# Kernel tuning notes

Hardware: AMD Instinct MI355X
Metric: run time of the kernel (lower is better)

## Reference

```python
import jax, jax.numpy as jnp
import numpy as np

B, S, D, H = 4, 2048, 1024, 16
HD = D // H


def setup_inputs() -> dict:
    key = jax.random.key(0)
    ks = jax.random.split(key, 12)
    inp = {
        'query': jax.random.normal(ks[0], (B, S, D), jnp.float32),
        'key': jax.random.normal(ks[1], (B, S, D), jnp.float32),
        'value': jax.random.normal(ks[2], (B, S, D), jnp.float32),
        'mask': jnp.ones((B, 1, 1, S), jnp.bool_),
        # nn.Linear weights are [out, in]; y = x @ W.T + b
        'Wq': jax.random.normal(ks[3], (D, D), jnp.float32) * 0.02,
        'bq': jnp.zeros((D,), jnp.float32),
        'Wk': jax.random.normal(ks[4], (D, D), jnp.float32) * 0.02,
        'bk': jnp.zeros((D,), jnp.float32),
        'Wv': jax.random.normal(ks[5], (D, D), jnp.float32) * 0.02,
        'bv': jnp.zeros((D,), jnp.float32),
        'Wo': jax.random.normal(ks[6], (D, D), jnp.float32) * 0.02,
        'bo': jnp.zeros((D,), jnp.float32),
    }
    return inp


def reference(query, key, value, mask, Wq, bq, Wk, bk, Wv, bv, Wo, bo):
    scale = 1.0 / np.sqrt(HD).astype(np.float32)

    def proj(x, W, b):
        # [B,S,D] -> [B,H,S,HD]
        y = x @ W.T + b
        return y.reshape(B, S, H, HD).transpose(0, 2, 1, 3)

    q = proj(query, Wq, bq)
    k = proj(key, Wk, bk)
    v = proj(value, Wv, bv)
    # scores: [B,H,S,S]
    scores = jnp.einsum('bhqd,bhkd->bhqk', q, k) * scale
    scores = jnp.where(mask, scores, -jnp.inf)
    attn = jax.nn.softmax(scores, axis=-1)  # dropout p=0 in eval
    ctx = jnp.einsum('bhqk,bhkd->bhqd', attn, v)  # [B,H,S,HD]
    ctx = ctx.transpose(0, 2, 1, 3).reshape(B, S, D)
    return ctx @ Wo.T + bo
```

## Files before the change

### kernel.cpp

```cpp
#include <hip/hip_runtime.h>
#include <hip/hip_bf16.h>

#define LOG2E 1.4426950408889634f
#define SCLOG (0.125f * 1.4426950408889634f)

typedef __attribute__((ext_vector_type(8))) short short8;
typedef __attribute__((ext_vector_type(4))) float f32x4;

__device__ __forceinline__ short f2bf(float f) {
    __hip_bfloat16 h = __float2bfloat16(f);
    short s;
    __builtin_memcpy(&s, &h, 2);
    return s;
}

__device__ __forceinline__ void gl_lds16(const void* g, void* l) {
    __builtin_amdgcn_global_load_lds(
        (const __attribute__((address_space(1))) unsigned int*)g,
        (__attribute__((address_space(3))) unsigned int*)l,
        16, 0, 0);
}

__global__ __launch_bounds__(256) void cvt3(
    const float* __restrict__ a, const float* __restrict__ b,
    const float* __restrict__ c, short* __restrict__ oa,
    short* __restrict__ ob, short* __restrict__ oc, int n8)
{
    int i = blockIdx.x * 256 + threadIdx.x;
    if (i >= n8) return;
    const float* in = blockIdx.y == 0 ? a : (blockIdx.y == 1 ? b : c);
    short* out = blockIdx.y == 0 ? oa : (blockIdx.y == 1 ? ob : oc);
    float4 v0 = ((const float4*)in)[2 * i];
    float4 v1 = ((const float4*)in)[2 * i + 1];
    short8 s = { f2bf(v0.x), f2bf(v0.y), f2bf(v0.z), f2bf(v0.w),
                 f2bf(v1.x), f2bf(v1.y), f2bf(v1.z), f2bf(v1.w) };
    *(short8*)(out + 8 * (size_t)i) = s;
}

__global__ __launch_bounds__(256) void cvt4(
    const float* __restrict__ a, const float* __restrict__ b,
    const float* __restrict__ c, const float* __restrict__ d,
    short* __restrict__ oa, short* __restrict__ ob,
    short* __restrict__ oc, short* __restrict__ od, int n8)
{
    int i = blockIdx.x * 256 + threadIdx.x;
    if (i >= n8) return;
    const float* in = blockIdx.y == 0 ? a : (blockIdx.y == 1 ? b :
                      (blockIdx.y == 2 ? c : d));
    short* out = blockIdx.y == 0 ? oa : (blockIdx.y == 1 ? ob :
                 (blockIdx.y == 2 ? oc : od));
    float4 v0 = ((const float4*)in)[2 * i];
    float4 v1 = ((const float4*)in)[2 * i + 1];
    short8 s = { f2bf(v0.x), f2bf(v0.y), f2bf(v0.z), f2bf(v0.w),
                 f2bf(v1.x), f2bf(v1.y), f2bf(v1.z), f2bf(v1.w) };
    *(short8*)(out + 8 * (size_t)i) = s;
}

template<int NZ, bool OUT_BF16>
__global__ __launch_bounds__(256) void gemm_bt_bf16(
    const short* __restrict__ A0, const short* __restrict__ A1,
    const short* __restrict__ A2,
    const short* __restrict__ W0, const short* __restrict__ W1,
    const short* __restrict__ W2,
    const float* __restrict__ b0, const float* __restrict__ b1,
    const float* __restrict__ b2,
    short* __restrict__ C0, short* __restrict__ C1, short* __restrict__ C2,
    void* __restrict__ Cf, int M, int N, int K)
{
    __shared__ short As[128 * 64];
    __shared__ short Bs[128 * 64];
    const int tid = threadIdx.x;
    const int wave = tid >> 6, lane = tid & 63;
    const int quad = lane >> 4, l16 = lane & 15;
    const int wm = (wave >> 1) * 64, wn = (wave & 1) * 64;
    const int bm0 = blockIdx.y * 128, bn0 = blockIdx.x * 128;
    const int rowA = lane >> 3;
    const int chunkS = (((lane & 7) ^ rowA) * 8);
    const int rsw = (l16 & 7);

    const short* A; const short* W; const float* bias; short* Cb;
    if constexpr (NZ == 3) {
        A    = blockIdx.z == 0 ? A0 : (blockIdx.z == 1 ? A1 : A2);
        W    = blockIdx.z == 0 ? W0 : (blockIdx.z == 1 ? W1 : W2);
        bias = blockIdx.z == 0 ? b0 : (blockIdx.z == 1 ? b1 : b2);
        Cb   = blockIdx.z == 0 ? C0 : (blockIdx.z == 1 ? C1 : C2);
    } else {
        A = A0; W = W0; bias = b0; Cb = C0;
    }

    const short* Ab = A + (size_t)bm0 * K;
    const short* Wb = W + (size_t)bn0 * K;

    f32x4 acc[4][4] = {};

    for (int kt = 0; kt < K; kt += 64) {
        #pragma unroll
        for (int i = 0; i < 4; ++i) {
            int r0 = wave * 32 + i * 8;
            gl_lds16(Ab + (size_t)(r0 + rowA) * K + kt + chunkS, As + r0 * 64);
            gl_lds16(Wb + (size_t)(r0 + rowA) * K + kt + chunkS, Bs + r0 * 64);
        }
        __syncthreads();

        #pragma unroll
        for (int h = 0; h < 2; ++h) {
            const int slot = ((h * 4 + quad) ^ rsw) * 8;
            short8 af[4], bf[4];
            #pragma unroll
            for (int mi = 0; mi < 4; ++mi)
                af[mi] = *(const short8*)(As + (wm + mi * 16 + l16) * 64 + slot);
            #pragma unroll
            for (int ni = 0; ni < 4; ++ni)
                bf[ni] = *(const short8*)(Bs + (wn + ni * 16 + l16) * 64 + slot);
            #pragma unroll
            for (int mi = 0; mi < 4; ++mi)
                #pragma unroll
                for (int ni = 0; ni < 4; ++ni)
                    acc[mi][ni] = __builtin_amdgcn_mfma_f32_16x16x32_bf16(
                        af[mi], bf[ni], acc[mi][ni], 0, 0, 0);
        }
        __syncthreads();
    }

    #pragma unroll
    for (int ni = 0; ni < 4; ++ni) {
        int n = bn0 + wn + ni * 16 + l16;
        float bb = bias[n];
        #pragma unroll
        for (int mi = 0; mi < 4; ++mi)
            #pragma unroll
            for (int r = 0; r < 4; ++r) {
                int m = bm0 + wm + mi * 16 + quad * 4 + r;
                float v = acc[mi][ni][r] + bb;
                if constexpr (OUT_BF16)
                    Cb[(size_t)m * N + n] = f2bf(v);
                else
                    ((float*)Cf)[(size_t)m * N + n] = v;
            }
    }
}

__global__ __launch_bounds__(256) void transpose_v(
    const short* __restrict__ Vb, short* __restrict__ VT)
{
    const int S = 2048, D = 1024;
    __shared__ short T[64 * 64];
    const int tid = threadIdx.x;
    const int s0 = blockIdx.x * 64;
    const int h  = blockIdx.y;
    const int b  = blockIdx.z;

    #pragma unroll
    for (int it = 0; it < 2; ++it) {
        int c = tid + it * 256;
        int s = c >> 3, cd = c & 7;
        short8 v = *(const short8*)(Vb + ((size_t)(b * S + s0 + s)) * D + h * 64 + cd * 8);
        int chunk = cd ^ ((s >> 3) & 7);
        *(short8*)(T + s * 64 + chunk * 8) = v;
    }
    __syncthreads();
    #pragma unroll
    for (int it = 0; it < 2; ++it) {
        int c = tid + it * 256;
        int d = c >> 3, so = (c & 7) * 8;
        short8 v;
        #pragma unroll
        for (int i = 0; i < 8; ++i) {
            int s = so + i;
            int chunk = (d >> 3) ^ ((s >> 3) & 7);
            v[i] = T[s * 64 + chunk * 8 + (d & 7)];
        }
        *(short8*)(VT + ((size_t)((b * 16 + h) * 64 + d)) * S + s0 + so) = v;
    }
}

__global__ __launch_bounds__(256) void flash_attn(
    const short* __restrict__ Q, const short* __restrict__ Kb,
    const short* __restrict__ VT, const int* __restrict__ mask,
    short* __restrict__ Ctx)
{
    const int S = 2048, D = 1024;
    __shared__ short Ks[64 * 64];
    __shared__ short Vs[64 * 64];
    __shared__ short Ps[4][32 * 72];

    const int tid = threadIdx.x;
    const int wave = tid >> 6, lane = tid & 63;
    const int quad = lane >> 4, l16 = lane & 15;
    const int q0 = blockIdx.x * 128 + wave * 32;
    const int head = blockIdx.y, b = blockIdx.z;
    const size_t qbase  = ((size_t)(b * S)) * D + head * 64;
    const size_t vtbase = ((size_t)((b * 16 + head) * 64)) * S;
    const int rowA = lane >> 3;
    const int chunkS = (((lane & 7) ^ rowA) * 8);
    const int rsw = (l16 & 7);

    short8 qf[2][2];
    #pragma unroll
    for (int qi = 0; qi < 2; ++qi)
        #pragma unroll
        for (int h = 0; h < 2; ++h)
            qf[qi][h] = *(const short8*)(Q + qbase + (size_t)(q0 + qi * 16 + l16) * D + h * 32 + quad * 8);

    f32x4 o[2][4] = {};
    float ls[2][4] = {};

    const int* mrow = mask + (size_t)b * S;
    short* Pw = Ps[wave];
    const int slot0 = (quad ^ rsw) * 8;
    const int slot1 = ((4 + quad) ^ rsw) * 8;

    for (int kt = 0; kt < S; kt += 64) {
        __syncthreads();
        {
            int r0 = wave * 16;
            gl_lds16(Kb + qbase + (size_t)(kt + r0 + rowA) * D + chunkS, Ks + r0 * 64);
            gl_lds16(Kb + qbase + (size_t)(kt + r0 + 8 + rowA) * D + chunkS, Ks + (r0 + 8) * 64);
            gl_lds16(VT + vtbase + (size_t)(r0 + rowA) * S + kt + chunkS, Vs + r0 * 64);
            gl_lds16(VT + vtbase + (size_t)(r0 + 8 + rowA) * S + kt + chunkS, Vs + (r0 + 8) * 64);
        }
        __syncthreads();

        float p[2][4][4];
        #pragma unroll
        for (int t = 0; t < 4; ++t) {
            short8 kf0 = *(const short8*)(Ks + (t * 16 + l16) * 64 + slot0);
            short8 kf1 = *(const short8*)(Ks + (t * 16 + l16) * 64 + slot1);
            float mb = mrow[kt + t * 16 + l16] != 0 ? 0.f : -1e30f;
            #pragma unroll
            for (int qi = 0; qi < 2; ++qi) {
                f32x4 a = {};
                a = __builtin_amdgcn_mfma_f32_16x16x32_bf16(qf[qi][0], kf0, a, 0, 0, 0);
                a = __builtin_amdgcn_mfma_f32_16x16x32_bf16(qf[qi][1], kf1, a, 0, 0, 0);
                #pragma unroll
                for (int r = 0; r < 4; ++r) {
                    float pv = __builtin_amdgcn_exp2f(__builtin_fmaf(a[r], SCLOG, mb));
                    p[qi][t][r] = pv;
                    ls[qi][r] += pv;
                }
            }
        }

        #pragma unroll
        for (int qi = 0; qi < 2; ++qi)
            #pragma unroll
            for (int t = 0; t < 4; ++t)
                #pragma unroll
                for (int r = 0; r < 4; ++r)
                    Pw[(qi * 16 + quad * 4 + r) * 72 + t * 16 + l16] = f2bf(p[qi][t][r]);

        #pragma unroll
        for (int h = 0; h < 2; ++h) {
            const int vslot = ((h * 4 + quad) ^ rsw) * 8;
            short8 pa0 = *(const short8*)(Pw + l16 * 72 + h * 32 + quad * 8);
            short8 pa1 = *(const short8*)(Pw + (16 + l16) * 72 + h * 32 + quad * 8);
            #pragma unroll
            for (int nt = 0; nt < 4; ++nt) {
                short8 bv = *(const short8*)(Vs + (nt * 16 + l16) * 64 + vslot);
                o[0][nt] = __builtin_amdgcn_mfma_f32_16x16x32_bf16(pa0, bv, o[0][nt], 0, 0, 0);
                o[1][nt] = __builtin_amdgcn_mfma_f32_16x16x32_bf16(pa1, bv, o[1][nt], 0, 0, 0);
            }
        }
    }

    #pragma unroll
    for (int qi = 0; qi < 2; ++qi)
        #pragma unroll
        for (int r = 0; r < 4; ++r) {
            float v = ls[qi][r];
            #pragma unroll
            for (int off = 1; off < 16; off <<= 1)
                v += __shfl_xor(v, off, 64);
            ls[qi][r] = 1.0f / v;
        }

    #pragma unroll
    for (int qi = 0; qi < 2; ++qi)
        #pragma unroll
        for (int nt = 0; nt < 4; ++nt)
            #pragma unroll
            for (int r = 0; r < 4; ++r) {
                float v = o[qi][nt][r] * ls[qi][r];
                Ctx[qbase + (size_t)(q0 + qi * 16 + quad * 4 + r) * D + nt * 16 + l16] = f2bf(v);
            }
}

extern "C" void kernel_launch(void* const* d_in, const int* in_sizes, int n_in,
                              void* d_out, int out_size, void* d_ws, size_t ws_size,
                              hipStream_t stream) {
    const int B = 4, S = 2048, D = 1024, H = 16;
    const int M = B * S;
    const size_t MD = (size_t)M * D;

    const float* q_in = (const float*)d_in[0];
    const float* k_in = (const float*)d_in[1];
    const float* v_in = (const float*)d_in[2];
    const int* mask = (const int*)d_in[3];
    const float* Wq = (const float*)d_in[4];
    const float* bq = (const float*)d_in[5];
    const float* Wk = (const float*)d_in[6];
    const float* bk = (const float*)d_in[7];
    const float* Wv = (const float*)d_in[8];
    const float* bv = (const float*)d_in[9];
    const float* Wo = (const float*)d_in[10];
    const float* bo = (const float*)d_in[11];

    short* S1 = (short*)d_ws;
    short* S2 = S1 + MD;
    short* S3 = S2 + MD;
    short* S4 = S3 + MD;
    short* wqb = S4 + MD;
    short* wkb = wqb + (size_t)D * D;
    short* wvb = wkb + (size_t)D * D;
    short* wob = wvb + (size_t)D * D;

    short *qbf = S1, *kbf = S2, *vbf = S3;
    short *Qb = S4, *Kb = S1, *Vb = S2, *VT = S3, *Ctx = S2;

    dim3 blk(256);
    int n8_in = (int)(MD / 8);
    int n8_w  = D * D / 8;
    cvt3<<<dim3((n8_in + 255) / 256, 3), blk, 0, stream>>>(
        q_in, k_in, v_in, qbf, kbf, vbf, n8_in);
    cvt4<<<dim3((n8_w + 255) / 256, 4), blk, 0, stream>>>(
        Wq, Wk, Wv, Wo, wqb, wkb, wvb, wob, n8_w);

    short* S5 = wob + (size_t)D * D;
    short* S6 = S5 + MD;
    short* Kb2 = S5;
    short* Vb2 = S6;
    dim3 g1(D / 128, M / 128, 3);
    gemm_bt_bf16<3, true><<<g1, blk, 0, stream>>>(
        qbf, kbf, vbf, wqb, wkb, wvb, bq, bk, bv,
        Qb, Kb2, Vb2, nullptr, M, D, D);

    transpose_v<<<dim3(S / 64, H, B), blk, 0, stream>>>(Vb2, VT);

    dim3 g2(S / 128, H, B);
    flash_attn<<<g2, blk, 0, stream>>>(Qb, Kb2, VT, mask, Ctx);

    dim3 g3(D / 128, M / 128, 1);
    gemm_bt_bf16<1, false><<<g3, blk, 0, stream>>>(
        Ctx, nullptr, nullptr, wob, nullptr, nullptr, bo, nullptr, nullptr,
        nullptr, nullptr, nullptr, (float*)d_out, M, D, D);
}
```

Measured before the change: 382.2 us.

## Double per-wave query rows in flash attention and swap QK^T MFMA operands

Each wave now handles 64 query rows instead of 32, with 256 rows per block, so every K/V tile loaded into LDS is reused across twice as many queries. The QK^T MFMA swaps its operands so each lane holds four consecutive keys for one query. That allows packed 8-byte P stores to LDS, a vectorized int4 mask load, and a scalar per-row sum that needs only two shuffles. The cost is more accumulator registers per wave (o grows to 4x4 f32x4) and half as many blocks, which may lower occupancy and SM fill.

Result: slower. 430.9 us (+12.8%).

```diff
diff --git a/kernel.cpp b/kernel.cpp
--- a/kernel.cpp
+++ b/kernel.cpp
@@ -182,33 +182,33 @@
     const int S = 2048, D = 1024;
     __shared__ short Ks[64 * 64];
     __shared__ short Vs[64 * 64];
-    __shared__ short Ps[4][32 * 72];
+    __shared__ short Ps[4][64 * 72];
 
     const int tid = threadIdx.x;
     const int wave = tid >> 6, lane = tid & 63;
     const int quad = lane >> 4, l16 = lane & 15;
-    const int q0 = blockIdx.x * 128 + wave * 32;
+    const int q0 = blockIdx.x * 256 + wave * 64;
     const int head = blockIdx.y, b = blockIdx.z;
     const size_t qbase  = ((size_t)(b * S)) * D + head * 64;
     const size_t vtbase = ((size_t)((b * 16 + head) * 64)) * S;
     const int rowA = lane >> 3;
     const int chunkS = (((lane & 7) ^ rowA) * 8);
     const int rsw = (l16 & 7);
-
-    short8 qf[2][2];
-    #pragma unroll
-    for (int qi = 0; qi < 2; ++qi)
+    const int slot0 = (quad ^ rsw) * 8;
+    const int slot1 = ((4 + quad) ^ rsw) * 8;
+
+    short8 qf[4][2];
+    #pragma unroll
+    for (int qi = 0; qi < 4; ++qi)
         #pragma unroll
         for (int h = 0; h < 2; ++h)
             qf[qi][h] = *(const short8*)(Q + qbase + (size_t)(q0 + qi * 16 + l16) * D + h * 32 + quad * 8);
 
-    f32x4 o[2][4] = {};
-    float ls[2][4] = {};
+    f32x4 o[4][4] = {};
+    float ls[4] = {};
 
     const int* mrow = mask + (size_t)b * S;
     short* Pw = Ps[wave];
-    const int slot0 = (quad ^ rsw) * 8;
-    const int slot1 = ((4 + quad) ^ rsw) * 8;
 
     for (int kt = 0; kt < S; kt += 64) {
         __syncthreads();
@@ -221,68 +221,74 @@
         }
         __syncthreads();
 
-        float p[2][4][4];
         #pragma unroll
         for (int t = 0; t < 4; ++t) {
             short8 kf0 = *(const short8*)(Ks + (t * 16 + l16) * 64 + slot0);
             short8 kf1 = *(const short8*)(Ks + (t * 16 + l16) * 64 + slot1);
-            float mb = mrow[kt + t * 16 + l16] != 0 ? 0.f : -1e30f;
-            #pragma unroll
-            for (int qi = 0; qi < 2; ++qi) {
+            int4 m4 = *(const int4*)(mrow + kt + t * 16 + quad * 4);
+            float mb0 = m4.x ? 0.f : -1e30f;
+            float mb1 = m4.y ? 0.f : -1e30f;
+            float mb2 = m4.z ? 0.f : -1e30f;
+            float mb3 = m4.w ? 0.f : -1e30f;
+            #pragma unroll
+            for (int qi = 0; qi < 4; ++qi) {
                 f32x4 a = {};
-                a = __builtin_amdgcn_mfma_f32_16x16x32_bf16(qf[qi][0], kf0, a, 0, 0, 0);
-                a = __builtin_amdgcn_mfma_f32_16x16x32_bf16(qf[qi][1], kf1, a, 0, 0, 0);
-                #pragma unroll
-                for (int r = 0; r < 4; ++r) {
-                    float pv = __builtin_amdgcn_exp2f(__builtin_fmaf(a[r], SCLOG, mb));
-                    p[qi][t][r] = pv;
-                    ls[qi][r] += pv;
-                }
+                a = __builtin_amdgcn_mfma_f32_16x16x32_bf16(kf0, qf[qi][0], a, 0, 0, 0);
+                a = __builtin_amdgcn_mfma_f32_16x16x32_bf16(kf1, qf[qi][1], a, 0, 0, 0);
+                float p0 = __builtin_amdgcn_exp2f(__builtin_fmaf(a[0], SCLOG, mb0));
+                float p1 = __builtin_amdgcn_exp2f(__builtin_fmaf(a[1], SCLOG, mb1));
+                float p2 = __builtin_amdgcn_exp2f(__builtin_fmaf(a[2], SCLOG, mb2));
+                float p3 = __builtin_amdgcn_exp2f(__builtin_fmaf(a[3], SCLOG, mb3));
+                ls[qi] += (p0 + p1) + (p2 + p3);
+                unsigned u0 = (unsigned)(unsigned short)f2bf(p0) |
+                              ((unsigned)(unsigned short)f2bf(p1) << 16);
+                unsigned u1 = (unsigned)(unsigned short)f2bf(p2) |
+                              ((unsigned)(unsigned short)f2bf(p3) << 16);
+                int2 pk; pk.x = (int)u0; pk.y = (int)u1;
+                *(int2*)(Pw + (qi * 16 + l16) * 72 + t * 16 + quad * 4) = pk;
             }
         }
-
-        #pragma unroll
-        for (int qi = 0; qi < 2; ++qi)
-            #pragma unroll
-            for (int t = 0; t < 4; ++t)
-                #pragma unroll
-                for (int r = 0; r < 4; ++r)
-                    Pw[(qi * 16 + quad * 4 + r) * 72 + t * 16 + l16] = f2bf(p[qi][t][r]);
 
         #pragma unroll
         for (int h = 0; h < 2; ++h) {
             const int vslot = ((h * 4 + quad) ^ rsw) * 8;
-            short8 pa0 = *(const short8*)(Pw + l16 * 72 + h * 32 + quad * 8);
-            short8 pa1 = *(const short8*)(Pw + (16 + l16) * 72 + h * 32 + quad * 8);
-            #pragma unroll
-            for (int nt = 0; nt < 4; ++nt) {
-                short8 bv = *(const short8*)(Vs + (nt * 16 + l16) * 64 + vslot);
-                o[0][nt] = __builtin_amdgcn_mfma_f32_16x16x32_bf16(pa0, bv, o[0][nt], 0, 0, 0);
-                o[1][nt] = __builtin_amdgcn_mfma_f32_16x16x32_bf16(pa1, bv, o[1][nt], 0, 0, 0);
+            short8 vv[4];
+            #pragma unroll
+            for (int nt = 0; nt < 4; ++nt)
+                vv[nt] = *(const short8*)(Vs + (nt * 16 + l16) * 64 + vslot);
+            #pragma unroll
+            for (int qi = 0; qi < 4; ++qi) {
+                short8 pa = *(const short8*)(Pw + (qi * 16 + l16) * 72 + h * 32 + quad * 8);
+                #pragma unroll
+                for (int nt = 0; nt < 4; ++nt)
+                    o[qi][nt] = __builtin_amdgcn_mfma_f32_16x16x32_bf16(pa, vv[nt], o[qi][nt], 0, 0, 0);
             }
         }
     }
 
-    #pragma unroll
-    for (int qi = 0; qi < 2; ++qi)
-        #pragma unroll
-        for (int r = 0; r < 4; ++r) {
-            float v = ls[qi][r];
-            #pragma unroll
-            for (int off = 1; off < 16; off <<= 1)
-                v += __shfl_xor(v, off, 64);
-            ls[qi][r] = 1.0f / v;
-        }
-
-    #pragma unroll
-    for (int qi = 0; qi < 2; ++qi)
+    float lsr[4];
+    #pragma unroll
+    for (int qi = 0; qi < 4; ++qi) {
+        float v = ls[qi];
+        v += __shfl_xor(v, 16, 64);
+        v += __shfl_xor(v, 32, 64);
+        lsr[qi] = v;
+    }
+
+    #pragma unroll
+    for (int qi = 0; qi < 4; ++qi) {
+        float linv[4];
+        #pragma unroll
+        for (int r = 0; r < 4; ++r)
+            linv[r] = 1.0f / __shfl(lsr[qi], quad * 4 + r, 64);
         #pragma unroll
         for (int nt = 0; nt < 4; ++nt)
             #pragma unroll
             for (int r = 0; r < 4; ++r) {
-                float v = o[qi][nt][r] * ls[qi][r];
+                float v = o[qi][nt][r] * linv[r];
                 Ctx[qbase + (size_t)(q0 + qi * 16 + quad * 4 + r) * D + nt * 16 + l16] = f2bf(v);
             }
+    }
 }
 
 extern "C" void kernel_launch(void* const* d_in, const int* in_sizes, int n_in,
@@ -313,9 +319,11 @@
     short* wkb = wqb + (size_t)D * D;
     short* wvb = wkb + (size_t)D * D;
     short* wob = wvb + (size_t)D * D;
+    short* S5 = wob + (size_t)D * D;
+    short* S6 = S5 + MD;
 
     short *qbf = S1, *kbf = S2, *vbf = S3;
-    short *Qb = S4, *Kb = S1, *Vb = S2, *VT = S3, *Ctx = S2;
+    short *Qb = S4, *Kb2 = S5, *Vb2 = S6, *VT = S3, *Ctx = S2;
 
     dim3 blk(256);
     int n8_in = (int)(MD / 8);
@@ -325,10 +333,6 @@
     cvt4<<<dim3((n8_w + 255) / 256, 4), blk, 0, stream>>>(
         Wq, Wk, Wv, Wo, wqb, wkb, wvb, wob, n8_w);
 
-    short* S5 = wob + (size_t)D * D;
-    short* S6 = S5 + MD;
-    short* Kb2 = S5;
-    short* Vb2 = S6;
     dim3 g1(D / 128, M / 128, 3);
     gemm_bt_bf16<3, true><<<g1, blk, 0, stream>>>(
         qbf, kbf, vbf, wqb, wkb, wvb, bq, bk, bv,
@@ -336,7 +340,7 @@
 
     transpose_v<<<dim3(S / 64, H, B), blk, 0, stream>>>(Vb2, VT);
 
-    dim3 g2(S / 128, H, B);
+    dim3 g2(S / 256, H, B);
     flash_attn<<<g2, blk, 0, stream>>>(Qb, Kb2, VT, mask, Ctx);
 
     dim3 g3(D / 128, M / 128, 1);
```
